# Performance work log

Hardware: AMD Instinct MI355X
Metric: run time of the kernel (lower is better)

Reference implementation:

```python
import jax, jax.numpy as jnp
import numpy as np
jax.config.update('jax_enable_x64', True)

B, S, D, H, V, P = 4, 2048, 512, 8, 100000, 256
NGRAMS = list(range(3, 9))  # n-gram lengths 3..8
DH = D // H
SCALE = np.float32(DH ** -0.5)

def _layernorm(x, g, b, eps=1e-5):
    m = jnp.mean(x, -1, keepdims=True)
    v = jnp.mean(jnp.square(x - m), -1, keepdims=True)
    return g * (x - m) / jnp.sqrt(v + eps) + b

def _mha(q, k, v, Wq, bq, Wk, bk, Wv, bv, Wo, bo):
    Bq, Lq, _ = q.shape
    qh = (q @ Wq + bq).reshape(Bq, Lq, H, DH)
    kh = (k @ Wk + bk).reshape(Bq, -1, H, DH)
    vh = (v @ Wv + bv).reshape(Bq, -1, H, DH)
    s = jnp.einsum('bqhd,bkhd->bhqk', qh, kh) * SCALE
    a = jax.nn.softmax(s, axis=-1)
    o = jnp.einsum('bhqk,bkhd->bqhd', a, vh).reshape(Bq, Lq, D)
    return o @ Wo + bo

def _ngram_hash(bytes_seq, n):
    # hash[:, i] = sum_k bytes[:, i-n+1+k] * 256**k for i >= n-1 else 0, then mod V
    # (int64 wraparound for n=8 matches torch semantics)
    b = bytes_seq.astype(jnp.int64)
    h = jnp.zeros_like(b)
    for k in range(n):
        shift = n - 1 - k
        shifted = jnp.pad(b, ((0, 0), (shift, 0)))[:, :S]
        h = h + shifted * (256 ** k)
    h = jnp.where(jnp.arange(S) >= (n - 1), h, 0)
    return h % V

def _forward(bytes_seq, patch_idx, byte_emb, ngram_emb, sWq, sbq, sWk, sbk, sWv, sbv, sWo, sbo, ln1g, ln1b, W1, b1, W2, b2, ln2g, ln2b, cWq, cbq, cWk, cbk, cWv, cbv, cWo, cbo):
    embeds = byte_emb[bytes_seq]  # [B,S,D]
    for j, n in enumerate(NGRAMS):
        embeds = embeds + ngram_emb[j][_ngram_hash(bytes_seq, n)]
    embeds = embeds / np.float32(len(NGRAMS) + 1)
    # one post-norm transformer encoder layer (relu FFN, eval mode / no dropout)
    x = _layernorm(embeds + _mha(embeds, embeds, embeds, sWq, sbq, sWk, sbk, sWv, sbv, sWo, sbo), ln1g, ln1b)
    ff = jax.nn.relu(x @ W1 + b1) @ W2 + b2
    x = _layernorm(x + ff, ln2g, ln2b)
    # gather patch-boundary queries per batch, cross-attend to full sequence
    q = jnp.take_along_axis(x, patch_idx[..., None], axis=1)  # [B,P,D]
    return _mha(q, x, x, cWq, cbq, cWk, cbk, cWv, cbv, cWo, cbo)

def setup_inputs():
    key = jax.random.key(0)
    ks = jax.random.split(key, 20)
    f32 = jnp.float32
    def rn(k, shape, scale=0.02):
        return (jax.random.normal(k, shape, f32) * scale).astype(f32)
    return {
        'bytes_seq': jax.random.randint(ks[0], (B, S), 0, 256, dtype=jnp.int64),
        'patch_idx': jnp.sort(jax.random.randint(ks[1], (B, P), 0, S, dtype=jnp.int64), axis=1),
        'byte_emb': rn(ks[2], (256, D)),
        'ngram_emb': rn(ks[3], (len(NGRAMS), V, D)),
        'sWq': rn(ks[4], (D, D)), 'sbq': jnp.zeros((D,), f32),
        'sWk': rn(ks[5], (D, D)), 'sbk': jnp.zeros((D,), f32),
        'sWv': rn(ks[6], (D, D)), 'sbv': jnp.zeros((D,), f32),
        'sWo': rn(ks[7], (D, D)), 'sbo': jnp.zeros((D,), f32),
        'ln1g': jnp.ones((D,), f32), 'ln1b': jnp.zeros((D,), f32),
        'W1': rn(ks[8], (D, 4 * D)), 'b1': jnp.zeros((4 * D,), f32),
        'W2': rn(ks[9], (4 * D, D)), 'b2': jnp.zeros((D,), f32),
        'ln2g': jnp.ones((D,), f32), 'ln2b': jnp.zeros((D,), f32),
        'cWq': rn(ks[10], (D, D)), 'cbq': jnp.zeros((D,), f32),
        'cWk': rn(ks[11], (D, D)), 'cbk': jnp.zeros((D,), f32),
        'cWv': rn(ks[12], (D, D)), 'cbv': jnp.zeros((D,), f32),
        'cWo': rn(ks[13], (D, D)), 'cbo': jnp.zeros((D,), f32),
    }

def reference(bytes_seq, patch_idx, byte_emb, ngram_emb, sWq, sbq, sWk, sbk, sWv, sbv, sWo, sbo, ln1g, ln1b, W1, b1, W2, b2, ln2g, ln2b, cWq, cbq, cWk, cbk, cWv, cbv, cWo, cbo):
    return _forward(bytes_seq, patch_idx, byte_emb, ngram_emb, sWq, sbq, sWk, sbk, sWv, sbv, sWo, sbo, ln1g, ln1b, W1, b1, W2, b2, ln2g, ln2b, cWq, cbq, cWk, cbk, cWv, cbv, cWo, cbo)
```

## Files before the change

### kernel.cpp

```cpp
#include <hip/hip_runtime.h>
#include <stdint.h>

#define B_   4
#define S_   2048
#define D_   512
#define H_   8
#define DH_  64
#define V_   100000
#define P_   256
#define N_   (B_*S_)
#define NP_  (B_*P_)

typedef _Float16 f16;
typedef _Float16 f16x8 __attribute__((ext_vector_type(8)));
typedef float    f32x4 __attribute__((ext_vector_type(4)));
typedef uint32_t u32x4 __attribute__((ext_vector_type(4)));

#define MFMA16(a,b,c) __builtin_amdgcn_mfma_f32_16x16x32_f16((a),(b),(c),0,0,0)
#define GLDS16(gp, lp) __builtin_amdgcn_global_load_lds( \
    (const __attribute__((address_space(1))) void*)(gp), \
    (__attribute__((address_space(3))) void*)(lp), 16, 0, 0)

struct WJobs {
  const float* src[10];
  f16* dst[10];
  int K[10], N[10], tiles[10];
};

__global__ __launch_bounds__(256) void prep_kernel(WJobs jobs,
    const float* __restrict__ sbq, const float* __restrict__ sbk,
    const float* __restrict__ sbv, const float* __restrict__ cbk,
    const float* __restrict__ cbv, float* __restrict__ bqkv,
    float* __restrict__ bckv,
    const int* __restrict__ bytes_seq, const float* __restrict__ byte_emb,
    const float* __restrict__ ngram_emb, f16* __restrict__ out16)
{
  int bid = blockIdx.x;
  if (bid < 10240) {
    const int j = bid >> 10, tile = bid & 1023;
    if (tile >= jobs.tiles[j]) return;
    const int K = jobs.K[j], N = jobs.N[j];
    const int ntiles = N >> 5;
    const int kt = (tile / ntiles) << 5, nt = (tile % ntiles) << 5;
    __shared__ float T[32][33];
    const int t = threadIdx.x;
    const float* src = jobs.src[j];
    #pragma unroll
    for (int p = 0; p < 4; p++) {
      int lin = t + p * 256;
      int rr = lin >> 5, cc = lin & 31;
      T[rr][cc] = src[(size_t)(kt + rr) * N + nt + cc];
    }
    __syncthreads();
    f16* dst = jobs.dst[j];
    #pragma unroll
    for (int p = 0; p < 4; p++) {
      int lin = t + p * 256;
      int rr = lin >> 5, cc = lin & 31;
      dst[(size_t)(nt + rr) * K + kt + cc] = (f16)T[cc][rr];
    }
    return;
  }
  bid -= 10240;
  if (bid < 10) {
    int t = bid * 256 + threadIdx.x;
    if (t < 512)       bqkv[t] = sbq[t];
    else if (t < 1024) bqkv[t] = sbk[t - 512];
    else if (t < 1536) bqkv[t] = sbv[t - 1024];
    else if (t < 2048) bckv[t - 1536] = cbk[t - 1536];
    else if (t < 2560) bckv[t - 1536] = cbv[t - 2048];
    return;
  }
  bid -= 10;
  const int pos = bid * 2 + (threadIdx.x >> 7);
  const int b = pos / S_, s = pos % S_;
  const int* bs = bytes_seq + (size_t)b * S_;

  int w[8];
  #pragma unroll
  for (int k = 0; k < 8; k++) {
    int p = s - 7 + k;
    w[k] = (p >= 0) ? bs[p] : 0;
  }
  int idx[6];
  #pragma unroll
  for (int j = 0; j < 6; j++) {
    const int n = j + 3;
    int id = 0;
    if (s >= n - 1) {
      uint64_t h = 0;
      for (int k = 0; k < n; k++)
        h += (uint64_t)(uint32_t)w[8 - n + k] << (8 * k);
      long long sh = (long long)h;
      long long r = sh % (long long)V_;
      if (r < 0) r += V_;
      id = (int)r;
    }
    idx[j] = id;
  }
  const int d = (threadIdx.x & 127) * 4;
  float4 acc = *(const float4*)(byte_emb + (size_t)bs[s] * D_ + d);
  #pragma unroll
  for (int j = 0; j < 6; j++) {
    const float4 v = *(const float4*)(ngram_emb + ((size_t)j * V_ + idx[j]) * D_ + d);
    acc.x += v.x; acc.y += v.y; acc.z += v.z; acc.w += v.w;
  }
  const float inv7 = 1.0f / 7.0f;
  f16 t4[4];
  t4[0] = (f16)(acc.x * inv7); t4[1] = (f16)(acc.y * inv7);
  t4[2] = (f16)(acc.z * inv7); t4[3] = (f16)(acc.w * inv7);
  *(uint2*)(out16 + (size_t)pos * D_ + d) = *(uint2*)t4;
}

template<typename OutT, int RELU, int BN, int VTSTART>
__device__ __forceinline__ void gemm_body(
    const f16* __restrict__ A, const f16* __restrict__ Bt,
    const float* __restrict__ bias, OutT* __restrict__ C,
    int M, int N, int K, const int* __restrict__ rowmap,
    f16* __restrict__ vt, int bmi, int bni)
{
  constexpr int NF = BN / 32;
  __shared__ __align__(16) f16 As[2][128 * 32];
  __shared__ __align__(16) f16 Bs[2][BN * 32];
  const int tid = threadIdx.x;
  const int l = tid & 63;
  const int lo4 = l & 15, hi2 = l >> 4;
  const int w = tid >> 6;
  const int wr = w >> 1, wc = w & 1;
  const int bm = bmi * 128, bn = bni * BN;

  size_t aoff[2];
  #pragma unroll
  for (int i = 0; i < 2; i++) {
    int r = bm + i * 64 + (tid >> 2);
    int ar = rowmap ? ((r >> 8) * S_ + rowmap[r]) : r;
    aoff[i] = (size_t)ar * K + (tid & 3) * 8;
  }

  f32x4 acc[4][NF];
  #pragma unroll
  for (int m = 0; m < 4; m++)
    #pragma unroll
    for (int n = 0; n < NF; n++) acc[m][n] = (f32x4){0.f, 0.f, 0.f, 0.f};

  const int nt = K >> 5;

  #pragma unroll
  for (int i = 0; i < 2; i++)
    GLDS16(A + aoff[i], &As[0][(i * 256 + tid) * 8]);
  #pragma unroll
  for (int i = 0; i < BN / 64; i++) {
    int c = i * 256 + tid;
    GLDS16(Bt + (size_t)(bn + (c >> 2)) * K + (c & 3) * 8, &Bs[0][c * 8]);
  }

  for (int t = 0; t < nt; t++) {
    __syncthreads();
    const int cur = t & 1;
    if (t + 1 < nt) {
      const int k0 = (t + 1) << 5;
      #pragma unroll
      for (int i = 0; i < 2; i++)
        GLDS16(A + aoff[i] + k0, &As[cur ^ 1][(i * 256 + tid) * 8]);
      #pragma unroll
      for (int i = 0; i < BN / 64; i++) {
        int c = i * 256 + tid;
        GLDS16(Bt + (size_t)(bn + (c >> 2)) * K + k0 + (c & 3) * 8, &Bs[cur ^ 1][c * 8]);
      }
    }
    f16x8 af[4], bf[NF];
    const f16* pa = &As[cur][(wr * 64 + lo4) * 32 + hi2 * 8];
    const f16* pb = &Bs[cur][(wc * (BN / 2) + lo4) * 32 + hi2 * 8];
    #pragma unroll
    for (int m = 0; m < 4; m++) af[m] = *(const f16x8*)(pa + m * 16 * 32);
    #pragma unroll
    for (int n = 0; n < NF; n++) bf[n] = *(const f16x8*)(pb + n * 16 * 32);
    #pragma unroll
    for (int m = 0; m < 4; m++)
      #pragma unroll
      for (int n = 0; n < NF; n++)
        acc[m][n] = MFMA16(af[m], bf[n], acc[m][n]);
  }

  if constexpr (VTSTART >= 0) {
    if (bn >= VTSTART) {
      #pragma unroll
      for (int n = 0; n < NF; n++) {
        const int col = bn + wc * (BN / 2) + n * 16 + lo4;
        const float bcol = bias[col];
        const int dcol = col - VTSTART;
        const size_t vbase = ((size_t)(dcol >> 6) * 64 + (dcol & 63)) << 11;
        #pragma unroll
        for (int m = 0; m < 4; m++) {
          const int row0 = bm + wr * 64 + m * 16 + hi2 * 4;
          f16 t4[4];
          #pragma unroll
          for (int j = 0; j < 4; j++) t4[j] = (f16)(acc[m][n][j] + bcol);
          *(uint2*)(vt + (((size_t)(row0 >> 11) * 8) << 17) + vbase + (row0 & 2047)) = *(uint2*)t4;
        }
      }
      return;
    }
  }

  #pragma unroll
  for (int n = 0; n < NF; n++) {
    const int col = bn + wc * (BN / 2) + n * 16 + lo4;
    const float bcol = bias[col];
    #pragma unroll
    for (int m = 0; m < 4; m++) {
      const int row0 = bm + wr * 64 + m * 16 + hi2 * 4;
      #pragma unroll
      for (int j = 0; j < 4; j++) {
        float v = acc[m][n][j] + bcol;
        if (RELU) v = fmaxf(v, 0.f);
        C[(size_t)(row0 + j) * N + col] = (OutT)v;
      }
    }
  }
}

template<typename OutT, int RELU, int BN, int VTSTART>
__global__ __launch_bounds__(256) void gemm_f16(
    const f16* __restrict__ A, const f16* __restrict__ Bt,
    const float* __restrict__ bias, OutT* __restrict__ C,
    int M, int N, int K, const int* __restrict__ rowmap, f16* __restrict__ vt)
{
  gemm_body<OutT, RELU, BN, VTSTART>(A, Bt, bias, C, M, N, K, rowmap, vt,
                                     blockIdx.x, blockIdx.y);
}

__global__ __launch_bounds__(256) void ckv_cq_kernel(
    const f16* __restrict__ X, const f16* __restrict__ CKVT,
    const float* __restrict__ bckv, f16* __restrict__ CKV,
    f16* __restrict__ vt2, const f16* __restrict__ cWqT,
    const float* __restrict__ cbq, f16* __restrict__ CQ,
    const int* __restrict__ pidx)
{
  int bid = blockIdx.x;
  if (bid < 512) {
    gemm_body<f16, 0, 128, 512>(X, CKVT, bckv, CKV, N_, 1024, 512,
                                nullptr, vt2, bid >> 3, bid & 7);
  } else {
    bid -= 512;
    gemm_body<f16, 0, 64, -1>(X, cWqT, cbq, CQ, NP_, 512, 512,
                              pidx, nullptr, bid >> 3, bid & 7);
  }
}

template<int QG>
__global__ __launch_bounds__(256) void attn_f16(
    const f16* __restrict__ Q, int qs,
    const f16* __restrict__ Kp, int kvs,
    const f16* __restrict__ VT, f16* __restrict__ O, int NQ)
{
  __shared__ __align__(16) f16 Ks[2][64][76];
  __shared__ __align__(16) f16 VtL[2][64 * 64];

  const int tid = threadIdx.x;
  const int w = tid >> 6, l = tid & 63;
  const int lo4 = l & 15, hi2 = l >> 4;
  const int lin = blockIdx.x;
  const int h = lin & 7, b = (lin >> 3) & 3, qt = lin >> 5;

  const f16 qscale = (f16)0.18033688f;
  f16x8 qf[QG][2];
  #pragma unroll
  for (int qg = 0; qg < QG; qg++) {
    const int qrow = qt * (64 * QG) + w * (16 * QG) + qg * 16 + lo4;
    const f16* Qp = Q + (size_t)(b * NQ + qrow) * qs + h * DH_ + hi2 * 8;
    qf[qg][0] = *(const f16x8*)(Qp);
    qf[qg][1] = *(const f16x8*)(Qp + 32);
    #pragma unroll
    for (int i = 0; i < 8; i++) { qf[qg][0][i] *= qscale; qf[qg][1][i] *= qscale; }
  }

  const int g2 = lo4 >> 2, j4 = lo4 & 3;
  const int kvp0 = 8 * g2 + j4;
  const int kvp1 = 8 * (g2 ^ 2) + 4 + j4;
  const int pidx = (l ^ 32) << 2;
  const int vswz = lo4 & 7;

  const f16* Kb = Kp + (size_t)b * S_ * kvs + h * DH_;
  const f16* VTbh = VT + (((size_t)(b * 8 + h)) << 17);

  float lsum[QG];
  f32x4 oacc[QG][4];
  #pragma unroll
  for (int qg = 0; qg < QG; qg++) {
    lsum[qg] = 0.f;
    #pragma unroll
    for (int df = 0; df < 4; df++) oacc[qg][df] = (f32x4){0.f, 0.f, 0.f, 0.f};
  }

  const int r0 = tid >> 3;
  const int c8 = tid & 7;
  const int vr = tid >> 3;
  const int vch = tid & 7;

  #pragma unroll
  for (int i = 0; i < 2; i++) {
    int r = i * 32 + vr, ch = vch;
    GLDS16(VTbh + (size_t)r * 2048 + ((ch ^ (r & 7)) * 8), &VtL[0][(i * 256 + tid) * 8]);
  }
  f16x8 kreg[2];
  #pragma unroll
  for (int i = 0; i < 2; i++)
    kreg[i] = *(const f16x8*)(Kb + (size_t)(i * 32 + r0) * kvs + c8 * 8);
  #pragma unroll
  for (int i = 0; i < 2; i++)
    *(f16x8*)(&Ks[0][i * 32 + r0][c8 * 8]) = kreg[i];
  __syncthreads();

  const int NT = S_ / 64;
  int cur = 0;
  for (int t = 0; t < NT; t++) {
    if (t + 1 < NT) {
      const int kt2 = (t + 1) * 64;
      #pragma unroll
      for (int i = 0; i < 2; i++) {
        int r = i * 32 + vr;
        GLDS16(VTbh + (size_t)r * 2048 + kt2 + ((vch ^ (r & 7)) * 8),
               &VtL[cur ^ 1][(i * 256 + tid) * 8]);
      }
      #pragma unroll
      for (int i = 0; i < 2; i++)
        kreg[i] = *(const f16x8*)(Kb + (size_t)(kt2 + i * 32 + r0) * kvs + c8 * 8);
    }
    f32x4 sacc[QG][4];
    #pragma unroll
    for (int nf = 0; nf < 4; nf++) {
      const int krow = ((nf & 1) ? kvp1 : kvp0) + (nf >> 1) * 32;
      f16x8 kf0 = *(const f16x8*)(&Ks[cur][krow][hi2 * 8]);
      f16x8 kf1 = *(const f16x8*)(&Ks[cur][krow][32 + hi2 * 8]);
      #pragma unroll
      for (int qg = 0; qg < QG; qg++) {
        f32x4 s = (f32x4){0.f, 0.f, 0.f, 0.f};
        s = MFMA16(kf0, qf[qg][0], s);
        s = MFMA16(kf1, qf[qg][1], s);
        sacc[qg][nf] = s;
      }
    }
    uint32_t packs[QG][4][2];
    #pragma unroll
    for (int qg = 0; qg < QG; qg++)
      #pragma unroll
      for (int nf = 0; nf < 4; nf++) {
        float p0 = exp2f(fminf(sacc[qg][nf][0], 15.f));
        float p1 = exp2f(fminf(sacc[qg][nf][1], 15.f));
        float p2 = exp2f(fminf(sacc[qg][nf][2], 15.f));
        float p3 = exp2f(fminf(sacc[qg][nf][3], 15.f));
        lsum[qg] += (p0 + p1) + (p2 + p3);
        packs[qg][nf][0] = __builtin_bit_cast(uint32_t, __builtin_amdgcn_cvt_pkrtz(p0, p1));
        packs[qg][nf][1] = __builtin_bit_cast(uint32_t, __builtin_amdgcn_cvt_pkrtz(p2, p3));
      }
    #pragma unroll
    for (int ks = 0; ks < 2; ks++) {
      f16x8 pb[QG];
      #pragma unroll
      for (int qg = 0; qg < QG; qg++) {
        uint32_t w0 = packs[qg][2 * ks][0];
        uint32_t w1 = packs[qg][2 * ks][1];
        uint32_t w2 = (uint32_t)__builtin_amdgcn_ds_bpermute(pidx, (int)packs[qg][2 * ks + 1][0]);
        uint32_t w3 = (uint32_t)__builtin_amdgcn_ds_bpermute(pidx, (int)packs[qg][2 * ks + 1][1]);
        u32x4 bw = (u32x4){w0, w1, w2, w3};
        pb[qg] = __builtin_bit_cast(f16x8, bw);
      }
      #pragma unroll
      for (int df = 0; df < 4; df++) {
        const int r = df * 16 + lo4;
        const int cc = (ks * 4 + hi2) ^ vswz;
        f16x8 vf = *(const f16x8*)(&VtL[cur][r * 64 + cc * 8]);
        #pragma unroll
        for (int qg = 0; qg < QG; qg++)
          oacc[qg][df] = MFMA16(vf, pb[qg], oacc[qg][df]);
      }
    }
    if (t + 1 < NT) {
      #pragma unroll
      for (int i = 0; i < 2; i++)
        *(f16x8*)(&Ks[cur ^ 1][i * 32 + r0][c8 * 8]) = kreg[i];
    }
    __syncthreads();
    cur ^= 1;
  }

  #pragma unroll
  for (int qg = 0; qg < QG; qg++) {
    float r = lsum[qg];
    r += __shfl_xor(r, 16, 64);
    r += __shfl_xor(r, 32, 64);
    const float invl = 1.0f / r;
    const int orow = qt * (64 * QG) + w * (16 * QG) + qg * 16 + lo4;
    f16* Ob = O + (size_t)(b * NQ + orow) * D_ + h * DH_ + hi2 * 4;
    #pragma unroll
    for (int df = 0; df < 4; df++) {
      f16 t4[4];
      #pragma unroll
      for (int j = 0; j < 4; j++) t4[j] = (f16)(oacc[qg][df][j] * invl);
      *(uint2*)(Ob + df * 16) = *(uint2*)t4;
    }
  }
}

__global__ __launch_bounds__(128) void ln_kernel(
    const f16* __restrict__ a, const f16* __restrict__ r,
    const float* __restrict__ g, const float* __restrict__ be,
    f16* __restrict__ out)
{
  const int row = blockIdx.x;
  const int t = threadIdx.x;
  const f16* ap = a + (size_t)row * D_ + t * 4;
  const f16* rp = r + (size_t)row * D_ + t * 4;
  uint2 au = *(const uint2*)ap, ru = *(const uint2*)rp;
  f16 a4[4], r4[4];
  *(uint2*)a4 = au; *(uint2*)r4 = ru;
  float x0 = (float)a4[0] + (float)r4[0];
  float x1 = (float)a4[1] + (float)r4[1];
  float x2 = (float)a4[2] + (float)r4[2];
  float x3 = (float)a4[3] + (float)r4[3];
  float sm = x0 + x1 + x2 + x3;
  float sq = x0*x0 + x1*x1 + x2*x2 + x3*x3;
  #pragma unroll
  for (int off = 32; off > 0; off >>= 1) {
    sm += __shfl_down(sm, off, 64);
    sq += __shfl_down(sq, off, 64);
  }
  __shared__ float s0[2], s1[2];
  if ((t & 63) == 0) { s0[t >> 6] = sm; s1[t >> 6] = sq; }
  __syncthreads();
  const float Sm = s0[0] + s0[1];
  const float Sq = s1[0] + s1[1];
  const float mean = Sm * (1.0f / 512.0f);
  const float var  = Sq * (1.0f / 512.0f) - mean * mean;
  const float inv  = rsqrtf(var + 1e-5f);
  const float4 vg = *(const float4*)(g + t * 4);
  const float4 vb = *(const float4*)(be + t * 4);
  f16 o4[4];
  o4[0] = (f16)(vg.x * (x0 - mean) * inv + vb.x);
  o4[1] = (f16)(vg.y * (x1 - mean) * inv + vb.y);
  o4[2] = (f16)(vg.z * (x2 - mean) * inv + vb.z);
  o4[3] = (f16)(vg.w * (x3 - mean) * inv + vb.w);
  *(uint2*)(out + (size_t)row * D_ + t * 4) = *(uint2*)o4;
}

extern "C" void kernel_launch(void* const* d_in, const int* in_sizes, int n_in,
                              void* d_out, int out_size, void* d_ws, size_t ws_size,
                              hipStream_t stream) {
  const int*   bytes_seq = (const int*)  d_in[0];
  const int*   patch_idx = (const int*)  d_in[1];
  const float* byte_emb  = (const float*)d_in[2];
  const float* ngram_emb = (const float*)d_in[3];
  const float* sWq = (const float*)d_in[4];  const float* sbq = (const float*)d_in[5];
  const float* sWk = (const float*)d_in[6];  const float* sbk = (const float*)d_in[7];
  const float* sWv = (const float*)d_in[8];  const float* sbv = (const float*)d_in[9];
  const float* sWo = (const float*)d_in[10]; const float* sbo = (const float*)d_in[11];
  const float* ln1g = (const float*)d_in[12]; const float* ln1b = (const float*)d_in[13];
  const float* W1 = (const float*)d_in[14];  const float* b1 = (const float*)d_in[15];
  const float* W2 = (const float*)d_in[16];  const float* b2 = (const float*)d_in[17];
  const float* ln2g = (const float*)d_in[18]; const float* ln2b = (const float*)d_in[19];
  const float* cWq = (const float*)d_in[20]; const float* cbq = (const float*)d_in[21];
  const float* cWk = (const float*)d_in[22]; const float* cbk = (const float*)d_in[23];
  const float* cWv = (const float*)d_in[24]; const float* cbv = (const float*)d_in[25];
  const float* cWo = (const float*)d_in[26]; const float* cbo = (const float*)d_in[27];

  char* base = (char*)d_ws;
  const size_t MB = 1u << 20;
  f16* E16     = (f16*)(base + 0 * MB);
  f16* TMP16   = (f16*)(base + 8 * MB);
  f16* X116    = (f16*)(base + 16 * MB);
  f16* X216    = (f16*)(base + 24 * MB);
  f16* QKV16   = (f16*)(base + 32 * MB);
  f16* AT16    = (f16*)(base + 56 * MB);
  f16* HID16   = (f16*)(base + 64 * MB);
  f16* CKV16   = (f16*)(base + 96 * MB);
  f16* CQ16    = (f16*)(base + 112 * MB);
  f16* CO16    = (f16*)(base + 113 * MB);
  f16* WT      = (f16*)(base + 114 * MB);
  float* bqkv  = (float*)(base + 123 * MB);
  float* bckv  = bqkv + 1536;
  f16* VT      = (f16*)(base + 124 * MB);
  f16* VT2     = (f16*)(base + 132 * MB);

  f16* QKVT = WT;
  f16* sWoT = QKVT + 786432;
  f16* W1T  = sWoT + 262144;
  f16* W2T  = W1T + 1048576;
  f16* cWqT = W2T + 1048576;
  f16* CKVT = cWqT + 262144;
  f16* cWoT = CKVT + 524288;

  WJobs wj;
  {
    const float* wsrc[10] = {sWq, sWk, sWv, sWo, W1, W2, cWq, cWk, cWv, cWo};
    f16* wdst[10] = {QKVT, QKVT + 262144, QKVT + 524288, sWoT, W1T, W2T,
                     cWqT, CKVT, CKVT + 262144, cWoT};
    const int wK[10] = {512,512,512,512, 512,2048, 512,512,512,512};
    const int wN[10] = {512,512,512,512, 2048,512, 512,512,512,512};
    for (int i = 0; i < 10; i++) {
      wj.src[i] = wsrc[i]; wj.dst[i] = wdst[i];
      wj.K[i] = wK[i]; wj.N[i] = wN[i];
      wj.tiles[i] = (wK[i] >> 5) * (wN[i] >> 5);
    }
  }

  const dim3 blk256(256), blk128(128);

  prep_kernel<<<10240 + 10 + 4096, blk256, 0, stream>>>(
      wj, sbq, sbk, sbv, cbk, cbv, bqkv, bckv,
      bytes_seq, byte_emb, ngram_emb, E16);

  gemm_f16<f16, 0, 128, 1024><<<dim3(64, 12), blk256, 0, stream>>>(
      E16, QKVT, bqkv, QKV16, N_, 1536, 512, nullptr, VT);

  attn_f16<2><<<512, blk256, 0, stream>>>(QKV16, 1536, QKV16 + 512, 1536, VT, AT16, S_);

  gemm_f16<f16, 0, 64, -1><<<dim3(64, 8), blk256, 0, stream>>>(
      AT16, sWoT, sbo, TMP16, N_, 512, 512, nullptr, nullptr);
  ln_kernel<<<N_, blk128, 0, stream>>>(E16, TMP16, ln1g, ln1b, X116);

  gemm_f16<f16, 1, 128, -1><<<dim3(64, 16), blk256, 0, stream>>>(
      X116, W1T, b1, HID16, N_, 2048, 512, nullptr, nullptr);
  gemm_f16<f16, 0, 64, -1><<<dim3(64, 8), blk256, 0, stream>>>(
      HID16, W2T, b2, TMP16, N_, 512, 2048, nullptr, nullptr);
  ln_kernel<<<N_, blk128, 0, stream>>>(X116, TMP16, ln2g, ln2b, X216);

  ckv_cq_kernel<<<576, blk256, 0, stream>>>(
      X216, CKVT, bckv, CKV16, VT2, cWqT, cbq, CQ16, patch_idx);
  attn_f16<1><<<128, blk256, 0, stream>>>(CQ16, 512, CKV16, 1024, VT2, CO16, P_);

  gemm_f16<float, 0, 64, -1><<<dim3(8, 8), blk256, 0, stream>>>(
      CO16, cWoT, cbo, (float*)d_out, NP_, 512, 512, nullptr, nullptr);
}
```

Before: 289.6 us.

## Split cross-attention over KV chunks, template GEMM K, pack two LN rows per block

Cross-attention over the patch queries now splits the 2048-long KV sequence into 4 chunks, so 512 blocks run instead of 128. Each block writes unnormalized fp32 partial outputs and row sums, and a new reduce kernel combines them. The GEMM K dimension becomes a compile-time template parameter with pointer precomputation and a partially unrolled k-loop, and layernorm handles two rows per 256-thread block. The exp2 clamp is removed, which risks overflow, and the chunk combine adds extra kernel launches and global traffic.

```diff
diff --git a/kernel.cpp b/kernel.cpp
--- a/kernel.cpp
+++ b/kernel.cpp
@@ -112,14 +112,15 @@
   *(uint2*)(out16 + (size_t)pos * D_ + d) = *(uint2*)t4;
 }
 
-template<typename OutT, int RELU, int BN, int VTSTART>
+template<typename OutT, int RELU, int BN, int VTSTART, int K>
 __device__ __forceinline__ void gemm_body(
     const f16* __restrict__ A, const f16* __restrict__ Bt,
     const float* __restrict__ bias, OutT* __restrict__ C,
-    int M, int N, int K, const int* __restrict__ rowmap,
+    int N, const int* __restrict__ rowmap,
     f16* __restrict__ vt, int bmi, int bni)
 {
   constexpr int NF = BN / 32;
+  constexpr int NT = K / 32;
   __shared__ __align__(16) f16 As[2][128 * 32];
   __shared__ __align__(16) f16 Bs[2][BN * 32];
   const int tid = threadIdx.x;
@@ -129,57 +130,61 @@
   const int wr = w >> 1, wc = w & 1;
   const int bm = bmi * 128, bn = bni * BN;
 
-  size_t aoff[2];
+  const f16* ap[2];
   #pragma unroll
   for (int i = 0; i < 2; i++) {
     int r = bm + i * 64 + (tid >> 2);
     int ar = rowmap ? ((r >> 8) * S_ + rowmap[r]) : r;
-    aoff[i] = (size_t)ar * K + (tid & 3) * 8;
-  }
-
-  f32x4 acc[4][NF];
-  #pragma unroll
-  for (int m = 0; m < 4; m++)
-    #pragma unroll
-    for (int n = 0; n < NF; n++) acc[m][n] = (f32x4){0.f, 0.f, 0.f, 0.f};
-
-  const int nt = K >> 5;
-
-  #pragma unroll
-  for (int i = 0; i < 2; i++)
-    GLDS16(A + aoff[i], &As[0][(i * 256 + tid) * 8]);
+    ap[i] = A + (size_t)ar * K + (tid & 3) * 8;
+  }
+  const f16* bp[BN / 64];
   #pragma unroll
   for (int i = 0; i < BN / 64; i++) {
     int c = i * 256 + tid;
-    GLDS16(Bt + (size_t)(bn + (c >> 2)) * K + (c & 3) * 8, &Bs[0][c * 8]);
-  }
-
-  for (int t = 0; t < nt; t++) {
-    __syncthreads();
-    const int cur = t & 1;
-    if (t + 1 < nt) {
-      const int k0 = (t + 1) << 5;
-      #pragma unroll
-      for (int i = 0; i < 2; i++)
-        GLDS16(A + aoff[i] + k0, &As[cur ^ 1][(i * 256 + tid) * 8]);
-      #pragma unroll
-      for (int i = 0; i < BN / 64; i++) {
-        int c = i * 256 + tid;
-        GLDS16(Bt + (size_t)(bn + (c >> 2)) * K + k0 + (c & 3) * 8, &Bs[cur ^ 1][c * 8]);
-      }
-    }
-    f16x8 af[4], bf[NF];
-    const f16* pa = &As[cur][(wr * 64 + lo4) * 32 + hi2 * 8];
-    const f16* pb = &Bs[cur][(wc * (BN / 2) + lo4) * 32 + hi2 * 8];
-    #pragma unroll
-    for (int m = 0; m < 4; m++) af[m] = *(const f16x8*)(pa + m * 16 * 32);
-    #pragma unroll
-    for (int n = 0; n < NF; n++) bf[n] = *(const f16x8*)(pb + n * 16 * 32);
-    #pragma unroll
-    for (int m = 0; m < 4; m++)
-      #pragma unroll
-      for (int n = 0; n < NF; n++)
-        acc[m][n] = MFMA16(af[m], bf[n], acc[m][n]);
+    bp[i] = Bt + (size_t)(bn + (c >> 2)) * K + (c & 3) * 8;
+  }
+
+  f32x4 acc[4][NF];
+  #pragma unroll
+  for (int m = 0; m < 4; m++)
+    #pragma unroll
+    for (int n = 0; n < NF; n++) acc[m][n] = (f32x4){0.f, 0.f, 0.f, 0.f};
+
+  #pragma unroll
+  for (int i = 0; i < 2; i++)
+    GLDS16(ap[i], &As[0][(i * 256 + tid) * 8]);
+  #pragma unroll
+  for (int i = 0; i < BN / 64; i++)
+    GLDS16(bp[i], &Bs[0][(i * 256 + tid) * 8]);
+
+  for (int to = 0; to < NT / 8; to++) {
+    #pragma unroll
+    for (int ti = 0; ti < 8; ti++) {
+      const int t = to * 8 + ti;
+      __syncthreads();
+      const int cur = t & 1;
+      if (t + 1 < NT) {
+        const int k0 = (t + 1) << 5;
+        #pragma unroll
+        for (int i = 0; i < 2; i++)
+          GLDS16(ap[i] + k0, &As[cur ^ 1][(i * 256 + tid) * 8]);
+        #pragma unroll
+        for (int i = 0; i < BN / 64; i++)
+          GLDS16(bp[i] + k0, &Bs[cur ^ 1][(i * 256 + tid) * 8]);
+      }
+      f16x8 af[4], bf[NF];
+      const f16* pa = &As[cur][(wr * 64 + lo4) * 32 + hi2 * 8];
+      const f16* pb = &Bs[cur][(wc * (BN / 2) + lo4) * 32 + hi2 * 8];
+      #pragma unroll
+      for (int m = 0; m < 4; m++) af[m] = *(const f16x8*)(pa + m * 16 * 32);
+      #pragma unroll
+      for (int n = 0; n < NF; n++) bf[n] = *(const f16x8*)(pb + n * 16 * 32);
+      #pragma unroll
+      for (int m = 0; m < 4; m++)
+        #pragma unroll
+        for (int n = 0; n < NF; n++)
+          acc[m][n] = MFMA16(af[m], bf[n], acc[m][n]);
+    }
   }
 
   if constexpr (VTSTART >= 0) {
@@ -220,14 +225,14 @@
   }
 }
 
-template<typename OutT, int RELU, int BN, int VTSTART>
+template<typename OutT, int RELU, int BN, int VTSTART, int K>
 __global__ __launch_bounds__(256) void gemm_f16(
     const f16* __restrict__ A, const f16* __restrict__ Bt,
     const float* __restrict__ bias, OutT* __restrict__ C,
-    int M, int N, int K, const int* __restrict__ rowmap, f16* __restrict__ vt)
-{
-  gemm_body<OutT, RELU, BN, VTSTART>(A, Bt, bias, C, M, N, K, rowmap, vt,
-                                     blockIdx.x, blockIdx.y);
+    int N, const int* __restrict__ rowmap, f16* __restrict__ vt)
+{
+  gemm_body<OutT, RELU, BN, VTSTART, K>(A, Bt, bias, C, N, rowmap, vt,
+                                        blockIdx.x, blockIdx.y);
 }
 
 __global__ __launch_bounds__(256) void ckv_cq_kernel(
@@ -239,28 +244,32 @@
 {
   int bid = blockIdx.x;
   if (bid < 512) {
-    gemm_body<f16, 0, 128, 512>(X, CKVT, bckv, CKV, N_, 1024, 512,
-                                nullptr, vt2, bid >> 3, bid & 7);
+    gemm_body<f16, 0, 128, 512, 512>(X, CKVT, bckv, CKV, 1024,
+                                     nullptr, vt2, bid >> 3, bid & 7);
   } else {
     bid -= 512;
-    gemm_body<f16, 0, 64, -1>(X, cWqT, cbq, CQ, NP_, 512, 512,
-                              pidx, nullptr, bid >> 3, bid & 7);
-  }
-}
-
-template<int QG>
+    gemm_body<f16, 0, 64, -1, 512>(X, cWqT, cbq, CQ, 512,
+                                   pidx, nullptr, bid >> 3, bid & 7);
+  }
+}
+
+template<int QG, int CHUNKS>
 __global__ __launch_bounds__(256) void attn_f16(
     const f16* __restrict__ Q, int qs,
     const f16* __restrict__ Kp, int kvs,
-    const f16* __restrict__ VT, f16* __restrict__ O, int NQ)
-{
+    const f16* __restrict__ VT, f16* __restrict__ O,
+    float* __restrict__ Opart, float* __restrict__ Lpart, int NQ)
+{
+  constexpr int CL = S_ / CHUNKS;
+  constexpr int NT = CL / 64;
   __shared__ __align__(16) f16 Ks[2][64][76];
   __shared__ __align__(16) f16 VtL[2][64 * 64];
 
   const int tid = threadIdx.x;
   const int w = tid >> 6, l = tid & 63;
   const int lo4 = l & 15, hi2 = l >> 4;
-  const int lin = blockIdx.x;
+  const int lin = (CHUNKS == 1) ? blockIdx.x : (blockIdx.x & 127);
+  const int c   = (CHUNKS == 1) ? 0 : (int)(blockIdx.x >> 7);
   const int h = lin & 7, b = (lin >> 3) & 3, qt = lin >> 5;
 
   const f16 qscale = (f16)0.18033688f;
@@ -281,8 +290,8 @@
   const int pidx = (l ^ 32) << 2;
   const int vswz = lo4 & 7;
 
-  const f16* Kb = Kp + (size_t)b * S_ * kvs + h * DH_;
-  const f16* VTbh = VT + (((size_t)(b * 8 + h)) << 17);
+  const f16* Kb = Kp + ((size_t)b * S_ + c * CL) * kvs + h * DH_;
+  const f16* VTbh = VT + (((size_t)(b * 8 + h)) << 17) + c * CL;
 
   float lsum[QG];
   f32x4 oacc[QG][4];
@@ -295,13 +304,11 @@
 
   const int r0 = tid >> 3;
   const int c8 = tid & 7;
-  const int vr = tid >> 3;
-  const int vch = tid & 7;
 
   #pragma unroll
   for (int i = 0; i < 2; i++) {
-    int r = i * 32 + vr, ch = vch;
-    GLDS16(VTbh + (size_t)r * 2048 + ((ch ^ (r & 7)) * 8), &VtL[0][(i * 256 + tid) * 8]);
+    int r = i * 32 + r0;
+    GLDS16(VTbh + (size_t)r * 2048 + ((c8 ^ (r & 7)) * 8), &VtL[0][(i * 256 + tid) * 8]);
   }
   f16x8 kreg[2];
   #pragma unroll
@@ -312,15 +319,14 @@
     *(f16x8*)(&Ks[0][i * 32 + r0][c8 * 8]) = kreg[i];
   __syncthreads();
 
-  const int NT = S_ / 64;
   int cur = 0;
   for (int t = 0; t < NT; t++) {
     if (t + 1 < NT) {
       const int kt2 = (t + 1) * 64;
       #pragma unroll
       for (int i = 0; i < 2; i++) {
-        int r = i * 32 + vr;
-        GLDS16(VTbh + (size_t)r * 2048 + kt2 + ((vch ^ (r & 7)) * 8),
+        int r = i * 32 + r0;
+        GLDS16(VTbh + (size_t)r * 2048 + kt2 + ((c8 ^ (r & 7)) * 8),
                &VtL[cur ^ 1][(i * 256 + tid) * 8]);
       }
       #pragma unroll
@@ -346,10 +352,10 @@
     for (int qg = 0; qg < QG; qg++)
       #pragma unroll
       for (int nf = 0; nf < 4; nf++) {
-        float p0 = exp2f(fminf(sacc[qg][nf][0], 15.f));
-        float p1 = exp2f(fminf(sacc[qg][nf][1], 15.f));
-        float p2 = exp2f(fminf(sacc[qg][nf][2], 15.f));
-        float p3 = exp2f(fminf(sacc[qg][nf][3], 15.f));
+        float p0 = exp2f(sacc[qg][nf][0]);
+        float p1 = exp2f(sacc[qg][nf][1]);
+        float p2 = exp2f(sacc[qg][nf][2]);
+        float p3 = exp2f(sacc[qg][nf][3]);
         lsum[qg] += (p0 + p1) + (p2 + p3);
         packs[qg][nf][0] = __builtin_bit_cast(uint32_t, __builtin_amdgcn_cvt_pkrtz(p0, p1));
         packs[qg][nf][1] = __builtin_bit_cast(uint32_t, __builtin_amdgcn_cvt_pkrtz(p2, p3));
@@ -390,26 +396,59 @@
     float r = lsum[qg];
     r += __shfl_xor(r, 16, 64);
     r += __shfl_xor(r, 32, 64);
-    const float invl = 1.0f / r;
     const int orow = qt * (64 * QG) + w * (16 * QG) + qg * 16 + lo4;
-    f16* Ob = O + (size_t)(b * NQ + orow) * D_ + h * DH_ + hi2 * 4;
-    #pragma unroll
-    for (int df = 0; df < 4; df++) {
-      f16 t4[4];
-      #pragma unroll
-      for (int j = 0; j < 4; j++) t4[j] = (f16)(oacc[qg][df][j] * invl);
-      *(uint2*)(Ob + df * 16) = *(uint2*)t4;
-    }
-  }
-}
-
-__global__ __launch_bounds__(128) void ln_kernel(
+    if constexpr (CHUNKS == 1) {
+      const float invl = 1.0f / r;
+      f16* Ob = O + (size_t)(b * NQ + orow) * D_ + h * DH_ + hi2 * 4;
+      #pragma unroll
+      for (int df = 0; df < 4; df++) {
+        f16 t4[4];
+        #pragma unroll
+        for (int j = 0; j < 4; j++) t4[j] = (f16)(oacc[qg][df][j] * invl);
+        *(uint2*)(Ob + df * 16) = *(uint2*)t4;
+      }
+    } else {
+      float* Op = Opart + ((size_t)c * NP_ + b * NQ + orow) * D_ + h * DH_ + hi2 * 4;
+      #pragma unroll
+      for (int df = 0; df < 4; df++) {
+        float4 v = {oacc[qg][df][0], oacc[qg][df][1], oacc[qg][df][2], oacc[qg][df][3]};
+        *(float4*)(Op + df * 16) = v;
+      }
+      if (hi2 == 0)
+        Lpart[((size_t)c * NP_ + b * NQ + orow) * H_ + h] = r;
+    }
+  }
+}
+
+__global__ __launch_bounds__(128) void attn_reduce(
+    const float* __restrict__ Opart, const float* __restrict__ Lpart,
+    f16* __restrict__ CO)
+{
+  const int row = blockIdx.x;
+  const int col = threadIdx.x * 4;
+  const int h = col >> 6;
+  float4 o = {0.f, 0.f, 0.f, 0.f};
+  float ls = 0.f;
+  #pragma unroll
+  for (int c = 0; c < 4; c++) {
+    const float4 v = *(const float4*)(Opart + ((size_t)c * NP_ + row) * D_ + col);
+    o.x += v.x; o.y += v.y; o.z += v.z; o.w += v.w;
+    ls += Lpart[((size_t)c * NP_ + row) * H_ + h];
+  }
+  const float inv = 1.0f / ls;
+  f16 t4[4];
+  t4[0] = (f16)(o.x * inv); t4[1] = (f16)(o.y * inv);
+  t4[2] = (f16)(o.z * inv); t4[3] = (f16)(o.w * inv);
+  *(uint2*)(CO + (size_t)row * D_ + col) = *(uint2*)t4;
+}
+
+__global__ __launch_bounds__(256) void ln_kernel(
     const f16* __restrict__ a, const f16* __restrict__ r,
     const float* __restrict__ g, const float* __restrict__ be,
     f16* __restrict__ out)
 {
-  const int row = blockIdx.x;
-  const int t = threadIdx.x;
+  const int row = blockIdx.x * 2 + (threadIdx.x >> 7);
+  const int t = threadIdx.x & 127;
   const f16* ap = a + (size_t)row * D_ + t * 4;
   const f16* rp = r + (size_t)row * D_ + t * 4;
   uint2 au = *(const uint2*)ap, ru = *(const uint2*)rp;
@@ -426,11 +465,12 @@
     sm += __shfl_down(sm, off, 64);
     sq += __shfl_down(sq, off, 64);
   }
-  __shared__ float s0[2], s1[2];
-  if ((t & 63) == 0) { s0[t >> 6] = sm; s1[t >> 6] = sq; }
+  __shared__ float s0[4], s1[4];
+  if ((threadIdx.x & 63) == 0) { s0[threadIdx.x >> 6] = sm; s1[threadIdx.x >> 6] = sq; }
   __syncthreads();
-  const float Sm = s0[0] + s0[1];
-  const float Sq = s1[0] + s1[1];
+  const int base = (threadIdx.x >> 7) * 2;
+  const float Sm = s0[base] + s0[base + 1];
+  const float Sq = s1[base] + s1[base + 1];
   const float mean = Sm * (1.0f / 512.0f);
   const float var  = Sq * (1.0f / 512.0f) - mean * mean;
   const float inv  = rsqrtf(var + 1e-5f);
@@ -481,6 +521,8 @@
   float* bckv  = bqkv + 1536;
   f16* VT      = (f16*)(base + 124 * MB);
   f16* VT2     = (f16*)(base + 132 * MB);
+  float* OPART = (float*)(base + 140 * MB);
+  float* LPART = (float*)(base + 148 * MB);
 
   f16* QKVT = WT;
   f16* sWoT = QKVT + 786432;
@@ -510,25 +552,28 @@
       wj, sbq, sbk, sbv, cbk, cbv, bqkv, bckv,
       bytes_seq, byte_emb, ngram_emb, E16);
 
-  gemm_f16<f16, 0, 128, 1024><<<dim3(64, 12), blk256, 0, stream>>>(
-      E16, QKVT, bqkv, QKV16, N_, 1536, 512, nullptr, VT);
-
-  attn_f16<2><<<512, blk256, 0, stream>>>(QKV16, 1536, QKV16 + 512, 1536, VT, AT16, S_);
-
-  gemm_f16<f16, 0, 64, -1><<<dim3(64, 8), blk256, 0, stream>>>(
-      AT16, sWoT, sbo, TMP16, N_, 512, 512, nullptr, nullptr);
-  ln_kernel<<<N_, blk128, 0, stream>>>(E16, TMP16, ln1g, ln1b, X116);
-
-  gemm_f16<f16, 1, 128, -1><<<dim3(64, 16), blk256, 0, stream>>>(
-      X116, W1T, b1, HID16, N_, 2048, 512, nullptr, nullptr);
-  gemm_f16<f16, 0, 64, -1><<<dim3(64, 8), blk256, 0, stream>>>(
-      HID16, W2T, b2, TMP16, N_, 512, 2048, nullptr, nullptr);
-  ln_kernel<<<N_, blk128, 0, stream>>>(X116, TMP16, ln2g, ln2b, X216);
+  gemm_f16<f16, 0, 128, 1024, 512><<<dim3(64, 12), blk256, 0, stream>>>(
+      E16, QKVT, bqkv, QKV16, 1536, nullptr, VT);
+
+  attn_f16<2, 1><<<512, blk256, 0, stream>>>(
+      QKV16, 1536, QKV16 + 512, 1536, VT, AT16, nullptr, nullptr, S_);
+
+  gemm_f16<f16, 0, 64, -1, 512><<<dim3(64, 8), blk256, 0, stream>>>(
+      AT16, sWoT, sbo, TMP16, 512, nullptr, nullptr);
+  ln_kernel<<<N_/2, blk256, 0, stream>>>(E16, TMP16, ln1g, ln1b, X116);
+
+  gemm_f16<f16, 1, 128, -1, 512><<<dim3(64, 16), blk256, 0, stream>>>(
+      X116, W1T, b1, HID16, 2048, nullptr, nullptr);
+  gemm_f16<f16, 0, 64, -1, 2048><<<dim3(64, 8), blk256, 0, stream>>>(
+      HID16, W2T, b2, TMP16, 512, nullptr, nullptr);
+  ln_kernel<<<N_/2, blk256, 0, stream>>>(X116, TMP16, ln2g, ln2b, X216);
 
   ckv_cq_kernel<<<576, blk256, 0, stream>>>(
       X216, CKVT, bckv, CKV16, VT2, cWqT, cbq, CQ16, patch_idx);
-  attn_f16<1><<<128, blk256, 0, stream>>>(CQ16, 512, CKV16, 1024, VT2, CO16, P_);
-
-  gemm_f16<float, 0, 64, -1><<<dim3(8, 8), blk256, 0, stream>>>(
-      CO16, cWoT, cbo, (float*)d_out, NP_, 512, 512, nullptr, nullptr);
-}
+  attn_f16<1, 4><<<512, blk256, 0, stream>>>(
+      CQ16, 512, CKV16, 1024, VT2, nullptr, OPART, LPART, P_);
+  attn_reduce<<<NP_, blk128, 0, stream>>>(OPART, LPART, CO16);
+
+  gemm_f16<float, 0, 64, -1, 512><<<dim3(8, 8), blk256, 0, stream>>>(
+      CO16, cWoT, cbo, (float*)d_out, 512, nullptr, nullptr);
+}
```

After: 278.9 us. 3.7% less time.
